# Kernel optimization log

Measured on AMD Instinct MI355X. Metric: run time of the kernel, lower is better.

Reference implementation:

```python
import jax, jax.numpy as jnp
import numpy as np

B, FDIM, H, E = 16384, 512, 256, 128  # batch, feature_dim, lstm hidden, scenario encoding


def setup_inputs() -> dict:
    key = jax.random.key(0)
    ks = jax.random.split(key, 24)
    p = lambda k, shape: (jax.random.normal(k, shape, jnp.float32) * 0.05)
    return {
        "base_timeline": jax.random.normal(ks[0], (B, FDIM), jnp.float32),
        "counterfactual_scenario": jax.random.normal(ks[1], (B, FDIM), jnp.float32),
        # scenario_encoder: Linear(512,256) -> ReLU -> Linear(256,128)
        "w_se1": p(ks[2], (256, FDIM)), "b_se1": p(ks[3], (256,)),
        "w_se2": p(ks[4], (E, 256)), "b_se2": p(ks[5], (E,)),
        # LSTM layer 0: input 128, hidden 256 (gate order i,f,g,o)
        "w_ih0": p(ks[6], (4 * H, E)), "w_hh0": p(ks[7], (4 * H, H)),
        "b_ih0": p(ks[8], (4 * H,)), "b_hh0": p(ks[9], (4 * H,)),
        # LSTM layer 1: input 256, hidden 256
        "w_ih1": p(ks[10], (4 * H, H)), "w_hh1": p(ks[11], (4 * H, H)),
        "b_ih1": p(ks[12], (4 * H,)), "b_hh1": p(ks[13], (4 * H,)),
        # outcome_modifier: Linear(384,256) -> ReLU -> Linear(256,512) -> Tanh
        "w_om1": p(ks[14], (256, H + E)), "b_om1": p(ks[15], (256,)),
        "w_om2": p(ks[16], (FDIM, 256)), "b_om2": p(ks[17], (FDIM,)),
        # probability_estimator: Linear(512,128) -> ReLU -> Linear(128,1) -> Sigmoid
        "w_pe1": p(ks[18], (E, FDIM)), "b_pe1": p(ks[19], (E,)),
        "w_pe2": p(ks[20], (1, E)), "b_pe2": p(ks[21], (1,)),
        "num_steps": 10,
    }


def _lstm_cell(x_pre, h, c, w_hh, b_hh):
    gates = x_pre + h @ w_hh.T + b_hh  # [B, 4H]
    i, f, g, o = jnp.split(gates, 4, axis=-1)
    c = jax.nn.sigmoid(f) * c + jax.nn.sigmoid(i) * jnp.tanh(g)
    h = jax.nn.sigmoid(o) * jnp.tanh(c)
    return h, c


def reference(base_timeline, counterfactual_scenario,
              w_se1, b_se1, w_se2, b_se2,
              w_ih0, w_hh0, b_ih0, b_hh0,
              w_ih1, w_hh1, b_ih1, b_hh1,
              w_om1, b_om1, w_om2, b_om2,
              w_pe1, b_pe1, w_pe2, b_pe2,
              num_steps):
    # scenario encoding [B, 128]
    s = jax.nn.relu(counterfactual_scenario @ w_se1.T + b_se1) @ w_se2.T + b_se2
    bsz = base_timeline.shape[0]
    h = w_hh0.shape[1]
    # LSTM layer-0 input is the same scenario encoding each step -> precompute
    x_pre0 = s @ w_ih0.T + b_ih0  # [B, 4H]

    def step(carry, _):
        cur, h0, c0, h1, c1 = carry
        h0, c0 = _lstm_cell(x_pre0, h0, c0, w_hh0, b_hh0)
        x1 = h0 @ w_ih1.T + b_ih1
        h1, c1 = _lstm_cell(x1, h1, c1, w_hh1, b_hh1)
        comb = jnp.concatenate([h1, s], axis=-1)  # [B, 384]
        mod = jnp.tanh(jax.nn.relu(comb @ w_om1.T + b_om1) @ w_om2.T + b_om2)
        nxt = cur + 0.1 * mod
        prob = jax.nn.sigmoid(jax.nn.relu(nxt @ w_pe1.T + b_pe1) @ w_pe2.T + b_pe2)
        return (nxt, h0, c0, h1, c1), (nxt, prob)

    z = jnp.zeros((bsz, h), base_timeline.dtype)
    (final, _, _, _, _), (states, probs) = jax.lax.scan(
        step, (base_timeline, z, z, z, z), None, length=num_steps)
    alternate_timeline = jnp.swapaxes(states, 0, 1)        # [B, num_steps, 512]
    timeline_probabilities = jnp.swapaxes(probs, 0, 1)     # [B, num_steps, 1]
    return alternate_timeline, timeline_probabilities, s, final
```

## Files before the change

kernel.cpp:

```cpp
#include <hip/hip_runtime.h>

typedef short bf16x8 __attribute__((ext_vector_type(8)));
typedef float f32x4 __attribute__((ext_vector_type(4)));

#define DEV __device__ __forceinline__

DEV short f2bf(float f) {
  union { float f; unsigned u; } v; v.f = f;
  unsigned r = v.u + 0x7FFFu + ((v.u >> 16) & 1u);
  return (short)(r >> 16);
}
DEV float bf2f(short s) {
  union { unsigned u; float f; } v; v.u = ((unsigned)(unsigned short)s) << 16;
  return v.f;
}
DEV float sigm(float x) { return 1.0f / (1.0f + __expf(-x)); }
DEV float tanh_(float x) {
  float a = fabsf(x);
  float e = __expf(-2.0f * a);
  float t = (1.0f - e) / (1.0f + e);
  return copysignf(t, x);
}

#define LDS_S    0
#define LDS_H0   16384
#define LDS_H1   49152
#define LDS_SLAB 81920
#define LDS_PROB 147456
#define LDS_SZ   149504

#define OFF_SE1 0
#define OFF_SE2 131072
#define OFF_W0  163840
#define OFF_W1  557056
#define OFF_OM1 1081344
#define OFF_OM2 1179648
#define OFF_PE1 1310720

__global__ void prep_frag(const float* __restrict__ srcA, const float* __restrict__ srcB,
                          short* __restrict__ dst, int N, int K, int ksplit)
{
  const int e = blockIdx.x * 256 + threadIdx.x;
  if (e >= N * K) return;
  const int f = e >> 9;
  const int rix = e & 511;
  const int lane = rix >> 3, j = rix & 7;
  const int KK = K >> 5;
  const int ntile = f / KK, kk = f - ntile * KK;
  const int n = ntile * 16 + (lane & 15);
  const int k = kk * 32 + ((lane >> 4) << 3) + j;
  float v;
  if (k < ksplit) v = srcA[(size_t)n * ksplit + k];
  else            v = srcB[(size_t)n * (K - ksplit) + (k - ksplit)];
  dst[e] = f2bf(v);
}

template<int NT, int MT>
DEV void zacc(f32x4 (&acc)[NT][MT]) {
  #pragma unroll
  for (int n = 0; n < NT; ++n)
    #pragma unroll
    for (int m = 0; m < MT; ++m)
      acc[n][m] = (f32x4){0.f, 0.f, 0.f, 0.f};
}

template<int KK, int NT, int MT>
DEV void mm_tiles(const char* sm, int aBase0, int aStride0, int splitKB,
                  int aBase1, int aStride1,
                  const short* __restrict__ wf, int ntBase, int ntStride,
                  f32x4 (&acc)[NT][MT], int lane)
{
  const int l15 = lane & 15, l4 = lane >> 4;
  const short* wp = wf + lane * 8;
  constexpr int TOT = KK * NT;
  constexpr int D = TOT < 8 ? TOT : 8;
  bf16x8 rb[D];
  #pragma unroll
  for (int f = 0; f < D; ++f) {
    const int kkf = f / NT, ntf = f % NT;
    rb[f] = *(const bf16x8*)(wp + (size_t)((ntBase + ntf * ntStride) * KK + kkf) * 512);
  }
  #pragma unroll
  for (int kk = 0; kk < KK; ++kk) {
    const int kb = kk * 64 + l4 * 16;
    bf16x8 a[MT];
    #pragma unroll
    for (int m = 0; m < MT; ++m) {
      const int r = m * 16 + l15;
      int off;
      if (kb < splitKB) off = aBase0 + r * aStride0 + (kb ^ ((r & 7) << 4));
      else              off = aBase1 + r * aStride1 + ((kb - splitKB) ^ ((r & 7) << 4));
      a[m] = *(const bf16x8*)(sm + off);
    }
    #pragma unroll
    for (int nt = 0; nt < NT; ++nt) {
      const int f = kk * NT + nt;
      const int slot = f % D;
      #pragma unroll
      for (int m = 0; m < MT; ++m)
        acc[nt][m] = __builtin_amdgcn_mfma_f32_16x16x32_bf16(a[m], rb[slot], acc[nt][m], 0, 0, 0);
      if (f + D < TOT) {
        const int f2 = f + D, kk2 = f2 / NT, nt2 = f2 % NT;
        rb[slot] = *(const bf16x8*)(wp + (size_t)((ntBase + nt2 * ntStride) * KK + kk2) * 512);
      }
    }
  }
}

DEV void lstm_ew(f32x4 (&acc)[4][4], f32x4 bv, unsigned (&cpk)[8], unsigned (&hp)[8])
{
  #pragma unroll
  for (int m = 0; m < 4; ++m)
    #pragma unroll
    for (int qh = 0; qh < 2; ++qh) {
      const int pi = m * 2 + qh;
      const unsigned oldc = cpk[pi];
      unsigned newc = 0, newh = 0;
      #pragma unroll
      for (int ql = 0; ql < 2; ++ql) {
        const int q = qh * 2 + ql;
        const float gi = acc[0][m][q] + bv[0];
        const float gf = acc[1][m][q] + bv[1];
        const float gg = acc[2][m][q] + bv[2];
        const float go = acc[3][m][q] + bv[3];
        const float cold = bf2f((short)((oldc >> (ql * 16)) & 0xFFFFu));
        const float c = sigm(gf) * cold + sigm(gi) * tanh_(gg);
        const float h = sigm(go) * tanh_(c);
        newc |= ((unsigned)(unsigned short)f2bf(c)) << (ql * 16);
        newh |= ((unsigned)(unsigned short)f2bf(h)) << (ql * 16);
      }
      cpk[pi] = newc;
      hp[pi] = newh;
    }
}

__global__ __launch_bounds__(1024, 4) void atg_main(
    const float* __restrict__ base, const float* __restrict__ cf,
    const float* __restrict__ b_se1, const float* __restrict__ b_se2,
    const float* __restrict__ b_ih0, const float* __restrict__ b_hh0,
    const float* __restrict__ b_ih1, const float* __restrict__ b_hh1,
    const float* __restrict__ b_om1, const float* __restrict__ b_om2,
    const float* __restrict__ b_pe1, const float* __restrict__ w_pe2,
    const float* __restrict__ b_pe2,
    const short* __restrict__ wsb,
    float* __restrict__ outStates, float* __restrict__ probs,
    float* __restrict__ outS, float* __restrict__ outFinal, int nsteps)
{
  __shared__ __align__(16) char sm[LDS_SZ];
  const int tid = threadIdx.x;
  const int lane = tid & 63, wid = tid >> 6;
  const int l15 = lane & 15, l4 = lane >> 4;
  const int row0 = blockIdx.x * 64;

  float curv[32];
  #pragma unroll
  for (int i = 0; i < 2; ++i)
    #pragma unroll
    for (int m = 0; m < 4; ++m)
      #pragma unroll
      for (int q = 0; q < 4; ++q)
        curv[i * 16 + m * 4 + q] =
            base[(size_t)(row0 + m * 16 + l4 * 4 + q) * 512 + (wid * 2 + i) * 16 + l15];

  {
    const int r = tid >> 4, ci = tid & 15;
    const float* src = cf + (size_t)(row0 + r) * 512;
    #pragma unroll
    for (int i = 0; i < 8; ++i) {
      const int c = ci * 4 + i * 64;
      const float4 v = *(const float4*)(src + c);
      short4 h; h.x = f2bf(v.x); h.y = f2bf(v.y); h.z = f2bf(v.z); h.w = f2bf(v.w);
      *(short4*)(sm + LDS_SLAB + r * 1024 + ((c * 2) ^ ((r & 7) << 4))) = h;
    }
  }
  __syncthreads();

  {
    f32x4 acc[1][4]; zacc(acc);
    mm_tiles<16, 1, 4>(sm, LDS_SLAB, 1024, 1 << 28, LDS_SLAB, 1024, wsb + OFF_SE1, wid, 1, acc, lane);
    const int cc = wid * 16 + l15;
    const float bv = b_se1[cc];
    #pragma unroll
    for (int m = 0; m < 4; ++m)
      #pragma unroll
      for (int q = 0; q < 4; ++q) {
        const int rr = m * 16 + l4 * 4 + q;
        const float u = fmaxf(acc[0][m][q] + bv, 0.0f);
        *(short*)(sm + LDS_H0 + rr * 512 + ((cc * 2) ^ ((rr & 7) << 4))) = f2bf(u);
      }
  }
  __syncthreads();

  if (wid < 8) {
    f32x4 acc[1][4]; zacc(acc);
    mm_tiles<8, 1, 4>(sm, LDS_H0, 512, 1 << 28, LDS_H0, 512, wsb + OFF_SE2, wid, 1, acc, lane);
    const int cc = wid * 16 + l15;
    const float bv = b_se2[cc];
    #pragma unroll
    for (int m = 0; m < 4; ++m)
      #pragma unroll
      for (int q = 0; q < 4; ++q) {
        const int rr = m * 16 + l4 * 4 + q;
        const float v = acc[0][m][q] + bv;
        __builtin_nontemporal_store(v, outS + (size_t)(row0 + rr) * 128 + cc);
        *(short*)(sm + LDS_S + rr * 256 + ((cc * 2) ^ ((rr & 7) << 4))) = f2bf(v);
      }
  }
  __syncthreads();
  #pragma unroll
  for (int i = 0; i < 4; ++i)
    *(f32x4*)(sm + LDS_H0 + tid * 64 + i * 16) = (f32x4){0.f, 0.f, 0.f, 0.f};
  __syncthreads();

  f32x4 b0v, b1v;
  #pragma unroll
  for (int g = 0; g < 4; ++g) {
    const int c = g * 256 + wid * 16 + l15;
    b0v[g] = b_ih0[c] + b_hh0[c];
    b1v[g] = b_ih1[c] + b_hh1[c];
  }
  const float bo1 = b_om1[wid * 16 + l15];
  float bo2[2];
  #pragma unroll
  for (int i = 0; i < 2; ++i) bo2[i] = b_om2[(wid * 2 + i) * 16 + l15];
  float bp1 = 0.f, w2v = 0.f;
  if (wid < 8) { bp1 = b_pe1[wid * 16 + l15]; w2v = w_pe2[wid * 16 + l15]; }

  unsigned c0[8], c1[8];
  #pragma unroll
  for (int i = 0; i < 8; ++i) { c0[i] = 0u; c1[i] = 0u; }

  for (int step = 0; step < nsteps; ++step) {
    unsigned hp[8];
    {
      f32x4 acc[4][4]; zacc(acc);
      mm_tiles<12, 4, 4>(sm, LDS_S, 256, 256, LDS_H0, 512, wsb + OFF_W0, wid, 16, acc, lane);
      lstm_ew(acc, b0v, c0, hp);
    }
    __syncthreads();
    #pragma unroll
    for (int m = 0; m < 4; ++m)
      #pragma unroll
      for (int q = 0; q < 4; ++q) {
        const int rr = m * 16 + l4 * 4 + q;
        const int cc = wid * 16 + l15;
        const unsigned v = hp[m * 2 + (q >> 1)] >> ((q & 1) * 16);
        *(short*)(sm + LDS_H0 + rr * 512 + ((cc * 2) ^ ((rr & 7) << 4))) = (short)v;
      }
    __syncthreads();
    {
      f32x4 acc[4][4]; zacc(acc);
      mm_tiles<16, 4, 4>(sm, LDS_H0, 512, 512, LDS_H1, 512, wsb + OFF_W1, wid, 16, acc, lane);
      lstm_ew(acc, b1v, c1, hp);
    }
    __syncthreads();
    #pragma unroll
    for (int m = 0; m < 4; ++m)
      #pragma unroll
      for (int q = 0; q < 4; ++q) {
        const int rr = m * 16 + l4 * 4 + q;
        const int cc = wid * 16 + l15;
        const unsigned v = hp[m * 2 + (q >> 1)] >> ((q & 1) * 16);
        *(short*)(sm + LDS_H1 + rr * 512 + ((cc * 2) ^ ((rr & 7) << 4))) = (short)v;
      }
    __syncthreads();
    {
      f32x4 acc[1][4]; zacc(acc);
      mm_tiles<12, 1, 4>(sm, LDS_H1, 512, 512, LDS_S, 256, wsb + OFF_OM1, wid, 1, acc, lane);
      const int cc = wid * 16 + l15;
      #pragma unroll
      for (int m = 0; m < 4; ++m)
        #pragma unroll
        for (int q = 0; q < 4; ++q) {
          const int rr = m * 16 + l4 * 4 + q;
          const float u = fmaxf(acc[0][m][q] + bo1, 0.0f);
          *(short*)(sm + LDS_SLAB + rr * 512 + ((cc * 2) ^ ((rr & 7) << 4))) = f2bf(u);
        }
    }
    __syncthreads();
    {
      f32x4 acc[2][4]; zacc(acc);
      mm_tiles<8, 2, 4>(sm, LDS_SLAB, 512, 1 << 28, LDS_SLAB, 512, wsb + OFF_OM2, wid * 2, 1, acc, lane);
      #pragma unroll
      for (int i = 0; i < 2; ++i) {
        const int cc = (wid * 2 + i) * 16 + l15;
        #pragma unroll
        for (int m = 0; m < 4; ++m)
          #pragma unroll
          for (int q = 0; q < 4; ++q) {
            const int rr = m * 16 + l4 * 4 + q;
            const int ci = i * 16 + m * 4 + q;
            const float nx = curv[ci] + 0.1f * tanh_(acc[i][m][q] + bo2[i]);
            curv[ci] = nx;
            __builtin_nontemporal_store(nx,
                outStates + ((size_t)(row0 + rr) * nsteps + step) * 512 + cc);
          }
      }
    }
    __syncthreads();
    #pragma unroll
    for (int i = 0; i < 2; ++i)
      #pragma unroll
      for (int m = 0; m < 4; ++m)
        #pragma unroll
        for (int q = 0; q < 4; ++q) {
          const int rr = m * 16 + l4 * 4 + q;
          const int cc = (wid * 2 + i) * 16 + l15;
          *(short*)(sm + LDS_SLAB + rr * 1024 + ((cc * 2) ^ ((rr & 7) << 4))) =
              f2bf(curv[i * 16 + m * 4 + q]);
        }
    __syncthreads();
    if (wid < 8) {
      f32x4 acc[1][4]; zacc(acc);
      mm_tiles<16, 1, 4>(sm, LDS_SLAB, 1024, 1 << 28, LDS_SLAB, 1024, wsb + OFF_PE1, wid, 1, acc, lane);
      float part[16];
      #pragma unroll
      for (int m = 0; m < 4; ++m)
        #pragma unroll
        for (int q = 0; q < 4; ++q)
          part[m * 4 + q] = fmaxf(acc[0][m][q] + bp1, 0.0f) * w2v;
      #pragma unroll
      for (int d = 1; d < 16; d <<= 1)
        #pragma unroll
        for (int i = 0; i < 16; ++i)
          part[i] += __shfl_xor(part[i], d);
      if (l15 == 0) {
        #pragma unroll
        for (int m = 0; m < 4; ++m)
          #pragma unroll
          for (int q = 0; q < 4; ++q)
            *(float*)(sm + LDS_PROB + (wid * 64 + m * 16 + l4 * 4 + q) * 4) = part[m * 4 + q];
      }
    }
    __syncthreads();
    if (tid < 64) {
      float ssum = b_pe2[0];
      #pragma unroll
      for (int w = 0; w < 8; ++w)
        ssum += *(const float*)(sm + LDS_PROB + (w * 64 + tid) * 4);
      const float p = 1.0f / (1.0f + __expf(-ssum));
      __builtin_nontemporal_store(p, probs + (size_t)(row0 + tid) * nsteps + step);
    }
  }

  #pragma unroll
  for (int i = 0; i < 2; ++i)
    #pragma unroll
    for (int m = 0; m < 4; ++m)
      #pragma unroll
      for (int q = 0; q < 4; ++q)
        __builtin_nontemporal_store(curv[i * 16 + m * 4 + q],
            outFinal + (size_t)(row0 + m * 16 + l4 * 4 + q) * 512 + (wid * 2 + i) * 16 + l15);
}

extern "C" void kernel_launch(void* const* d_in, const int* in_sizes, int n_in,
                              void* d_out, int out_size, void* d_ws, size_t ws_size,
                              hipStream_t stream)
{
  const float* base  = (const float*)d_in[0];
  const float* cf    = (const float*)d_in[1];
  const float* w_se1 = (const float*)d_in[2];
  const float* b_se1 = (const float*)d_in[3];
  const float* w_se2 = (const float*)d_in[4];
  const float* b_se2 = (const float*)d_in[5];
  const float* w_ih0 = (const float*)d_in[6];
  const float* w_hh0 = (const float*)d_in[7];
  const float* b_ih0 = (const float*)d_in[8];
  const float* b_hh0 = (const float*)d_in[9];
  const float* w_ih1 = (const float*)d_in[10];
  const float* w_hh1 = (const float*)d_in[11];
  const float* b_ih1 = (const float*)d_in[12];
  const float* b_hh1 = (const float*)d_in[13];
  const float* w_om1 = (const float*)d_in[14];
  const float* b_om1 = (const float*)d_in[15];
  const float* w_om2 = (const float*)d_in[16];
  const float* b_om2 = (const float*)d_in[17];
  const float* w_pe1 = (const float*)d_in[18];
  const float* b_pe1 = (const float*)d_in[19];
  const float* w_pe2 = (const float*)d_in[20];
  const float* b_pe2 = (const float*)d_in[21];

  const int B = in_sizes[0] / 512;
  const long nsteps = ((long)out_size - (long)B * 640) / ((long)B * 513);
  short* wsb = (short*)d_ws;
  float* out = (float*)d_out;

  auto prep = [&](const float* A, const float* Bp, long off, int N, int K, int ks) {
    const int total = N * K;
    prep_frag<<<dim3((total + 255) / 256), dim3(256), 0, stream>>>(A, Bp, wsb + off, N, K, ks);
  };
  prep(w_se1, w_se1, OFF_SE1, 256, 512, 512);
  prep(w_se2, w_se2, OFF_SE2, 128, 256, 256);
  prep(w_ih0, w_hh0, OFF_W0, 1024, 384, 128);
  prep(w_ih1, w_hh1, OFF_W1, 1024, 512, 256);
  prep(w_om1, w_om1, OFF_OM1, 256, 384, 384);
  prep(w_om2, w_om2, OFF_OM2, 512, 256, 256);
  prep(w_pe1, w_pe1, OFF_PE1, 128, 512, 512);

  float* probs = out + (size_t)B * nsteps * 512;
  float* outS  = out + (size_t)B * nsteps * 513;
  float* outF  = outS + (size_t)B * 128;
  atg_main<<<dim3(B / 64), dim3(1024), 0, stream>>>(base, cf, b_se1, b_se2, b_ih0, b_hh0,
      b_ih1, b_hh1, b_om1, b_om2, b_pe1, w_pe2, b_pe2, wsb, out, probs, outS, outF, (int)nsteps);
}
```

Measured before the change: 3.105 ms.

## Halve block to 8 waves with two tiles per wave and coalesced state stores

Shrinks the workgroup from 1024 to 512 threads so each wave computes two LSTM gate tiles and more output tiles, reusing A fragments across N tiles and cutting idle waves in the narrow GEMMs. State outputs are now written as coalesced float4 stores read back from the bf16 LDS copy, rather than strided scalar stores from registers. This rounds the stored timelines to bf16 precision and raises register pressure per thread, which may hurt occupancy.

```diff
diff --git a/kernel.cpp b/kernel.cpp
--- a/kernel.cpp
+++ b/kernel.cpp
@@ -134,7 +134,7 @@
     }
 }
 
-__global__ __launch_bounds__(1024, 4) void atg_main(
+__global__ __launch_bounds__(512, 2) void atg_main(
     const float* __restrict__ base, const float* __restrict__ cf,
     const float* __restrict__ b_se1, const float* __restrict__ b_se2,
     const float* __restrict__ b_ih0, const float* __restrict__ b_hh0,
@@ -152,22 +152,22 @@
   const int l15 = lane & 15, l4 = lane >> 4;
   const int row0 = blockIdx.x * 64;
 
-  float curv[32];
-  #pragma unroll
-  for (int i = 0; i < 2; ++i)
+  float curv[64];
+  #pragma unroll
+  for (int i = 0; i < 4; ++i)
     #pragma unroll
     for (int m = 0; m < 4; ++m)
       #pragma unroll
       for (int q = 0; q < 4; ++q)
         curv[i * 16 + m * 4 + q] =
-            base[(size_t)(row0 + m * 16 + l4 * 4 + q) * 512 + (wid * 2 + i) * 16 + l15];
+            base[(size_t)(row0 + m * 16 + l4 * 4 + q) * 512 + (wid * 4 + i) * 16 + l15];
 
   {
-    const int r = tid >> 4, ci = tid & 15;
+    const int r = tid >> 3, ci = tid & 7;
     const float* src = cf + (size_t)(row0 + r) * 512;
     #pragma unroll
-    for (int i = 0; i < 8; ++i) {
-      const int c = ci * 4 + i * 64;
+    for (int i = 0; i < 16; ++i) {
+      const int c = ci * 4 + i * 32;
       const float4 v = *(const float4*)(src + c);
       short4 h; h.x = f2bf(v.x); h.y = f2bf(v.y); h.z = f2bf(v.z); h.w = f2bf(v.w);
       *(short4*)(sm + LDS_SLAB + r * 1024 + ((c * 2) ^ ((r & 7) << 4))) = h;
@@ -176,24 +176,27 @@
   __syncthreads();
 
   {
+    f32x4 acc[2][4]; zacc(acc);
+    mm_tiles<16, 2, 4>(sm, LDS_SLAB, 1024, 1 << 28, LDS_SLAB, 1024, wsb + OFF_SE1, wid * 2, 1, acc, lane);
+    #pragma unroll
+    for (int nt = 0; nt < 2; ++nt) {
+      const int cc = (wid * 2 + nt) * 16 + l15;
+      const float bv = b_se1[cc];
+      #pragma unroll
+      for (int m = 0; m < 4; ++m)
+        #pragma unroll
+        for (int q = 0; q < 4; ++q) {
+          const int rr = m * 16 + l4 * 4 + q;
+          const float u = fmaxf(acc[nt][m][q] + bv, 0.0f);
+          *(short*)(sm + LDS_H1 + rr * 512 + ((cc * 2) ^ ((rr & 7) << 4))) = f2bf(u);
+        }
+    }
+  }
+  __syncthreads();
+
+  {
     f32x4 acc[1][4]; zacc(acc);
-    mm_tiles<16, 1, 4>(sm, LDS_SLAB, 1024, 1 << 28, LDS_SLAB, 1024, wsb + OFF_SE1, wid, 1, acc, lane);
-    const int cc = wid * 16 + l15;
-    const float bv = b_se1[cc];
-    #pragma unroll
-    for (int m = 0; m < 4; ++m)
-      #pragma unroll
-      for (int q = 0; q < 4; ++q) {
-        const int rr = m * 16 + l4 * 4 + q;
-        const float u = fmaxf(acc[0][m][q] + bv, 0.0f);
-        *(short*)(sm + LDS_H0 + rr * 512 + ((cc * 2) ^ ((rr & 7) << 4))) = f2bf(u);
-      }
-  }
-  __syncthreads();
-
-  if (wid < 8) {
-    f32x4 acc[1][4]; zacc(acc);
-    mm_tiles<8, 1, 4>(sm, LDS_H0, 512, 1 << 28, LDS_H0, 512, wsb + OFF_SE2, wid, 1, acc, lane);
+    mm_tiles<8, 1, 4>(sm, LDS_H1, 512, 1 << 28, LDS_H1, 512, wsb + OFF_SE2, wid, 1, acc, lane);
     const int cc = wid * 16 + l15;
     const float bv = b_se2[cc];
     #pragma unroll
@@ -208,111 +211,130 @@
   }
   __syncthreads();
   #pragma unroll
-  for (int i = 0; i < 4; ++i)
-    *(f32x4*)(sm + LDS_H0 + tid * 64 + i * 16) = (f32x4){0.f, 0.f, 0.f, 0.f};
+  for (int i = 0; i < 8; ++i)
+    *(f32x4*)(sm + LDS_H0 + tid * 128 + i * 16) = (f32x4){0.f, 0.f, 0.f, 0.f};
   __syncthreads();
 
-  f32x4 b0v, b1v;
-  #pragma unroll
-  for (int g = 0; g < 4; ++g) {
-    const int c = g * 256 + wid * 16 + l15;
-    b0v[g] = b_ih0[c] + b_hh0[c];
-    b1v[g] = b_ih1[c] + b_hh1[c];
-  }
-  const float bo1 = b_om1[wid * 16 + l15];
-  float bo2[2];
-  #pragma unroll
-  for (int i = 0; i < 2; ++i) bo2[i] = b_om2[(wid * 2 + i) * 16 + l15];
-  float bp1 = 0.f, w2v = 0.f;
-  if (wid < 8) { bp1 = b_pe1[wid * 16 + l15]; w2v = w_pe2[wid * 16 + l15]; }
-
-  unsigned c0[8], c1[8];
-  #pragma unroll
-  for (int i = 0; i < 8; ++i) { c0[i] = 0u; c1[i] = 0u; }
+  unsigned c0[16], c1[16];
+  #pragma unroll
+  for (int i = 0; i < 16; ++i) { c0[i] = 0u; c1[i] = 0u; }
 
   for (int step = 0; step < nsteps; ++step) {
-    unsigned hp[8];
-    {
+    unsigned hp[2][8];
+    #pragma unroll
+    for (int js = 0; js < 2; ++js) {
       f32x4 acc[4][4]; zacc(acc);
-      mm_tiles<12, 4, 4>(sm, LDS_S, 256, 256, LDS_H0, 512, wsb + OFF_W0, wid, 16, acc, lane);
-      lstm_ew(acc, b0v, c0, hp);
-    }
-    __syncthreads();
-    #pragma unroll
-    for (int m = 0; m < 4; ++m)
-      #pragma unroll
-      for (int q = 0; q < 4; ++q) {
-        const int rr = m * 16 + l4 * 4 + q;
-        const int cc = wid * 16 + l15;
-        const unsigned v = hp[m * 2 + (q >> 1)] >> ((q & 1) * 16);
-        *(short*)(sm + LDS_H0 + rr * 512 + ((cc * 2) ^ ((rr & 7) << 4))) = (short)v;
-      }
-    __syncthreads();
-    {
-      f32x4 acc[4][4]; zacc(acc);
-      mm_tiles<16, 4, 4>(sm, LDS_H0, 512, 512, LDS_H1, 512, wsb + OFF_W1, wid, 16, acc, lane);
-      lstm_ew(acc, b1v, c1, hp);
-    }
-    __syncthreads();
-    #pragma unroll
-    for (int m = 0; m < 4; ++m)
-      #pragma unroll
-      for (int q = 0; q < 4; ++q) {
-        const int rr = m * 16 + l4 * 4 + q;
-        const int cc = wid * 16 + l15;
-        const unsigned v = hp[m * 2 + (q >> 1)] >> ((q & 1) * 16);
-        *(short*)(sm + LDS_H1 + rr * 512 + ((cc * 2) ^ ((rr & 7) << 4))) = (short)v;
-      }
-    __syncthreads();
-    {
-      f32x4 acc[1][4]; zacc(acc);
-      mm_tiles<12, 1, 4>(sm, LDS_H1, 512, 512, LDS_S, 256, wsb + OFF_OM1, wid, 1, acc, lane);
-      const int cc = wid * 16 + l15;
+      mm_tiles<12, 4, 4>(sm, LDS_S, 256, 256, LDS_H0, 512, wsb + OFF_W0, wid * 2 + js, 16, acc, lane);
+      f32x4 bv;
+      #pragma unroll
+      for (int g = 0; g < 4; ++g) {
+        const int c = g * 256 + (wid * 2 + js) * 16 + l15;
+        bv[g] = b_ih0[c] + b_hh0[c];
+      }
+      lstm_ew(acc, bv, *(unsigned(*)[8])&c0[js * 8], hp[js]);
+    }
+    __syncthreads();
+    #pragma unroll
+    for (int js = 0; js < 2; ++js)
       #pragma unroll
       for (int m = 0; m < 4; ++m)
         #pragma unroll
         for (int q = 0; q < 4; ++q) {
           const int rr = m * 16 + l4 * 4 + q;
-          const float u = fmaxf(acc[0][m][q] + bo1, 0.0f);
-          *(short*)(sm + LDS_SLAB + rr * 512 + ((cc * 2) ^ ((rr & 7) << 4))) = f2bf(u);
+          const int cc = (wid * 2 + js) * 16 + l15;
+          const unsigned v = hp[js][m * 2 + (q >> 1)] >> ((q & 1) * 16);
+          *(short*)(sm + LDS_H0 + rr * 512 + ((cc * 2) ^ ((rr & 7) << 4))) = (short)v;
         }
-    }
+    __syncthreads();
+    #pragma unroll
+    for (int js = 0; js < 2; ++js) {
+      f32x4 acc[4][4]; zacc(acc);
+      mm_tiles<16, 4, 4>(sm, LDS_H0, 512, 512, LDS_H1, 512, wsb + OFF_W1, wid * 2 + js, 16, acc, lane);
+      f32x4 bv;
+      #pragma unroll
+      for (int g = 0; g < 4; ++g) {
+        const int c = g * 256 + (wid * 2 + js) * 16 + l15;
+        bv[g] = b_ih1[c] + b_hh1[c];
+      }
+      lstm_ew(acc, bv, *(unsigned(*)[8])&c1[js * 8], hp[js]);
+    }
+    __syncthreads();
+    #pragma unroll
+    for (int js = 0; js < 2; ++js)
+      #pragma unroll
+      for (int m = 0; m < 4; ++m)
+        #pragma unroll
+        for (int q = 0; q < 4; ++q) {
+          const int rr = m * 16 + l4 * 4 + q;
+          const int cc = (wid * 2 + js) * 16 + l15;
+          const unsigned v = hp[js][m * 2 + (q >> 1)] >> ((q & 1) * 16);
+          *(short*)(sm + LDS_H1 + rr * 512 + ((cc * 2) ^ ((rr & 7) << 4))) = (short)v;
+        }
     __syncthreads();
     {
       f32x4 acc[2][4]; zacc(acc);
-      mm_tiles<8, 2, 4>(sm, LDS_SLAB, 512, 1 << 28, LDS_SLAB, 512, wsb + OFF_OM2, wid * 2, 1, acc, lane);
-      #pragma unroll
-      for (int i = 0; i < 2; ++i) {
-        const int cc = (wid * 2 + i) * 16 + l15;
+      mm_tiles<12, 2, 4>(sm, LDS_H1, 512, 512, LDS_S, 256, wsb + OFF_OM1, wid * 2, 1, acc, lane);
+      #pragma unroll
+      for (int nt = 0; nt < 2; ++nt) {
+        const int cc = (wid * 2 + nt) * 16 + l15;
+        const float bo1 = b_om1[cc];
         #pragma unroll
         for (int m = 0; m < 4; ++m)
           #pragma unroll
           for (int q = 0; q < 4; ++q) {
             const int rr = m * 16 + l4 * 4 + q;
-            const int ci = i * 16 + m * 4 + q;
-            const float nx = curv[ci] + 0.1f * tanh_(acc[i][m][q] + bo2[i]);
-            curv[ci] = nx;
-            __builtin_nontemporal_store(nx,
-                outStates + ((size_t)(row0 + rr) * nsteps + step) * 512 + cc);
+            const float u = fmaxf(acc[nt][m][q] + bo1, 0.0f);
+            *(short*)(sm + LDS_SLAB + rr * 512 + ((cc * 2) ^ ((rr & 7) << 4))) = f2bf(u);
           }
       }
     }
     __syncthreads();
-    #pragma unroll
-    for (int i = 0; i < 2; ++i)
+    {
+      f32x4 acc[4][4]; zacc(acc);
+      mm_tiles<8, 4, 4>(sm, LDS_SLAB, 512, 1 << 28, LDS_SLAB, 512, wsb + OFF_OM2, wid * 4, 1, acc, lane);
+      #pragma unroll
+      for (int i = 0; i < 4; ++i) {
+        const float bo2 = b_om2[(wid * 4 + i) * 16 + l15];
+        #pragma unroll
+        for (int m = 0; m < 4; ++m)
+          #pragma unroll
+          for (int q = 0; q < 4; ++q)
+            curv[i * 16 + m * 4 + q] += 0.1f * tanh_(acc[i][m][q] + bo2);
+      }
+    }
+    __syncthreads();
+    #pragma unroll
+    for (int i = 0; i < 4; ++i)
       #pragma unroll
       for (int m = 0; m < 4; ++m)
         #pragma unroll
         for (int q = 0; q < 4; ++q) {
           const int rr = m * 16 + l4 * 4 + q;
-          const int cc = (wid * 2 + i) * 16 + l15;
+          const int cc = (wid * 4 + i) * 16 + l15;
           *(short*)(sm + LDS_SLAB + rr * 1024 + ((cc * 2) ^ ((rr & 7) << 4))) =
               f2bf(curv[i * 16 + m * 4 + q]);
         }
     __syncthreads();
-    if (wid < 8) {
+    {
+      const int cc = wid * 16 + l15;
+      const float bp1 = b_pe1[cc];
+      const float w2v = w_pe2[cc];
       f32x4 acc[1][4]; zacc(acc);
       mm_tiles<16, 1, 4>(sm, LDS_SLAB, 1024, 1 << 28, LDS_SLAB, 1024, wsb + OFF_PE1, wid, 1, acc, lane);
+
+      #pragma unroll
+      for (int j = 0; j < 16; ++j) {
+        const int pos = tid * 4 + j * 2048;
+        const int r = pos >> 9, c = pos & 511;
+        const short4 hv = *(const short4*)(sm + LDS_SLAB + r * 1024 + ((c * 2) ^ ((r & 7) << 4)));
+        f32x4 f;
+        f[0] = bf2f(hv.x); f[1] = bf2f(hv.y); f[2] = bf2f(hv.z); f[3] = bf2f(hv.w);
+        __builtin_nontemporal_store(f,
+            (f32x4*)(outStates + ((size_t)(row0 + r) * nsteps + step) * 512 + c));
+        if (step == nsteps - 1)
+          __builtin_nontemporal_store(f, (f32x4*)(outFinal + (size_t)(row0 + r) * 512 + c));
+      }
+
       float part[16];
       #pragma unroll
       for (int m = 0; m < 4; ++m)
@@ -342,15 +364,6 @@
       __builtin_nontemporal_store(p, probs + (size_t)(row0 + tid) * nsteps + step);
     }
   }
-
-  #pragma unroll
-  for (int i = 0; i < 2; ++i)
-    #pragma unroll
-    for (int m = 0; m < 4; ++m)
-      #pragma unroll
-      for (int q = 0; q < 4; ++q)
-        __builtin_nontemporal_store(curv[i * 16 + m * 4 + q],
-            outFinal + (size_t)(row0 + m * 16 + l4 * 4 + q) * 512 + (wid * 2 + i) * 16 + l15);
 }
 
 extern "C" void kernel_launch(void* const* d_in, const int* in_sizes, int n_in,
@@ -400,6 +413,6 @@
   float* probs = out + (size_t)B * nsteps * 512;
   float* outS  = out + (size_t)B * nsteps * 513;
   float* outF  = outS + (size_t)B * 128;
-  atg_main<<<dim3(B / 64), dim3(1024), 0, stream>>>(base, cf, b_se1, b_se2, b_ih0, b_hh0,
+  atg_main<<<dim3(B / 64), dim3(512), 0, stream>>>(base, cf, b_se1, b_se2, b_ih0, b_hh0,
       b_ih1, b_hh1, b_om1, b_om2, b_pe1, w_pe2, b_pe2, wsb, out, probs, outS, outF, (int)nsteps);
 }
```

After: 3.846 ms. 23.9% more time.
